# Performance work log

Hardware: AMD Instinct MI355X
Metric: run time of the kernel (lower is better)

## Reference

```python
import jax, jax.numpy as jnp
import numpy as np

B, D, L = 4, 64, 4096  # batch, pos feature dim (=pos_learnable_dim), sequence length

def setup_inputs() -> dict:
    key = jax.random.key(0)
    k1, k2 = jax.random.split(key, 2)
    pos_embed = jax.random.normal(k1, (B, D, L), dtype=jnp.float32)
    # _LinearWithBias(D, D): torch weight [out, in], bias [out]
    W_pos = (jax.random.normal(k2, (D, D), dtype=jnp.float32) / np.float32(np.sqrt(D)))
    b_pos = jnp.zeros((D,), dtype=jnp.float32)
    SOFTPLUS0 = 0.6931472  # softplus(0) = ln 2, gpytorch default raw param -> constrained value
    lengthscale = jnp.asarray(SOFTPLUS0, dtype=jnp.float32)   # RBFKernel lengthscale
    outputscale = jnp.asarray(SOFTPLUS0, dtype=jnp.float32)   # ScaleKernel outputscale
    return {"pos_embed": pos_embed, "W_pos": W_pos, "b_pos": b_pos,
            "lengthscale": lengthscale, "outputscale": outputscale}

def reference(pos_embed, W_pos, b_pos, lengthscale, outputscale):
    # pos_embed: [B, D, L]
    x = jnp.swapaxes(pos_embed, 1, 2)          # [B, L, D] (transpose, linear, transpose back, transpose again)
    x = x @ W_pos.T + b_pos                    # learnable positional linear on feature dim
    # gpytorch ScaleKernel(RBFKernel): outputscale * exp(-0.5 * ||(x_i - x_j)/lengthscale||^2)
    xs = x / lengthscale                       # [B, L, D]
    sq = jnp.sum(xs * xs, axis=-1)             # [B, L]
    sq_dist = sq[:, :, None] + sq[:, None, :] - 2.0 * jnp.einsum('bld,bmd->blm', xs, xs)
    sq_dist = jnp.maximum(sq_dist, 0.0)        # gpytorch clamps sq dist at 0
    return outputscale * jnp.exp(-0.5 * sq_dist)  # [B, L, L]
```

## Files before the change

kernel.cpp:

```cpp
#include <hip/hip_runtime.h>

using bf16x8 = __attribute__((ext_vector_type(8))) __bf16;
using f32x16 = __attribute__((ext_vector_type(16))) float;

#define BB 4
#define DD 64
#define LL 4096

__global__ __launch_bounds__(256) void prep_kernel(
    const float* __restrict__ pe,
    const float* __restrict__ W,
    const float* __restrict__ bias,
    const float* __restrict__ ls,
    __bf16* __restrict__ xs,
    float* __restrict__ h)
{
    __shared__ float pe_lds[DD][64];
    __shared__ float W_lds[DD * DD];
    __shared__ float hpart[4][64];

    const int tid = threadIdx.x;
    const int blk = blockIdx.x;
    const int b  = blk >> 6;
    const int l0 = (blk & 63) * 64;

    {
        const int l = tid & 63;
        const int kb = tid >> 6;
        #pragma unroll
        for (int it = 0; it < 16; ++it) {
            const int k = it * 4 + kb;
            pe_lds[k][l] = pe[((size_t)b * DD + k) * LL + l0 + l];
        }
    }
    #pragma unroll
    for (int it = 0; it < 16; ++it)
        W_lds[it * 256 + tid] = W[it * 256 + tid];
    __syncthreads();

    const int w = tid >> 6;
    const int l = tid & 63;
    const float inv_ls = 1.0f / ls[0];

    float acc[16];
    #pragma unroll
    for (int i = 0; i < 16; ++i) acc[i] = bias[w * 16 + i];

    for (int k4 = 0; k4 < 16; ++k4) {
        const float p0 = pe_lds[k4 * 4 + 0][l];
        const float p1 = pe_lds[k4 * 4 + 1][l];
        const float p2 = pe_lds[k4 * 4 + 2][l];
        const float p3 = pe_lds[k4 * 4 + 3][l];
        #pragma unroll
        for (int i = 0; i < 16; ++i) {
            const float4 wv = *(const float4*)&W_lds[(w * 16 + i) * DD + k4 * 4];
            acc[i] += p0 * wv.x + p1 * wv.y + p2 * wv.z + p3 * wv.w;
        }
    }

    unsigned short out16[16];
    float hs = 0.0f;
    #pragma unroll
    for (int i = 0; i < 16; ++i) {
        const float xf = acc[i] * inv_ls;
        const __bf16 bv = (__bf16)xf;
        const float xr = (float)bv;
        hs += xr * xr;
        out16[i] = __builtin_bit_cast(unsigned short, bv);
    }
    {
        __bf16* dst = xs + ((size_t)b * LL + l0 + l) * DD + w * 16;
        *(uint4*)dst       = *(const uint4*)&out16[0];
        *(uint4*)(dst + 8) = *(const uint4*)&out16[8];
    }
    hpart[w][l] = hs;
    __syncthreads();
    if (tid < 64) {
        const float s = hpart[0][tid] + hpart[1][tid] + hpart[2][tid] + hpart[3][tid];
        h[(size_t)b * LL + l0 + tid] = 0.5f * s;
    }
}

__global__ __launch_bounds__(256) void gram_kernel(
    const __bf16* __restrict__ xs,
    const float* __restrict__ h,
    const float* __restrict__ osc,
    float* __restrict__ out)
{
    const int bid = blockIdx.x;
    const int b  = bid >> 10;
    const int t  = bid & 1023;
    const int ti = t >> 5, tj = t & 31;

    const int tid  = threadIdx.x;
    const int wid  = tid >> 6;
    const int lane = tid & 63;
    const int lr = lane & 31, lg = lane >> 5;

    const int rows0 = ti * 128 + (wid >> 1) * 64;
    const int cols0 = tj * 128 + (wid & 1) * 64;

    const __bf16* xsb = xs + (size_t)b * LL * DD;
    const float*  hb  = h + (size_t)b * LL;

    bf16x8 af[2][4], bg[2][4];
    #pragma unroll
    for (int mt = 0; mt < 2; ++mt)
        #pragma unroll
        for (int kk = 0; kk < 4; ++kk)
            af[mt][kk] = *(const bf16x8*)(xsb + (size_t)(rows0 + mt * 32 + lr) * DD + kk * 16 + lg * 8);
    #pragma unroll
    for (int nt = 0; nt < 2; ++nt)
        #pragma unroll
        for (int kk = 0; kk < 4; ++kk)
            bg[nt][kk] = *(const bf16x8*)(xsb + (size_t)(cols0 + nt * 32 + lr) * DD + kk * 16 + lg * 8);

    f32x16 acc[2][2];
    #pragma unroll
    for (int mt = 0; mt < 2; ++mt)
        #pragma unroll
        for (int nt = 0; nt < 2; ++nt)
            acc[mt][nt] = (f32x16)(0.0f);

    #pragma unroll
    for (int kk = 0; kk < 4; ++kk)
        #pragma unroll
        for (int mt = 0; mt < 2; ++mt)
            #pragma unroll
            for (int nt = 0; nt < 2; ++nt)
                acc[mt][nt] = __builtin_amdgcn_mfma_f32_32x32x16_bf16(
                    af[mt][kk], bg[nt][kk], acc[mt][nt], 0, 0, 0);

    const float c = osc[0];
    const float LOG2E = 1.4426950408889634f;

    #pragma unroll
    for (int mt = 0; mt < 2; ++mt) {
        float hi[16];
        #pragma unroll
        for (int r = 0; r < 16; ++r)
            hi[r] = hb[rows0 + mt * 32 + (r & 3) + 8 * (r >> 2) + 4 * lg];
        #pragma unroll
        for (int nt = 0; nt < 2; ++nt) {
            const int col = cols0 + nt * 32 + lr;
            const float hj = hb[col];
            #pragma unroll
            for (int r = 0; r < 16; ++r) {
                const int row = rows0 + mt * 32 + (r & 3) + 8 * (r >> 2) + 4 * lg;
                float tt = acc[mt][nt][r] - hi[r] - hj;
                tt = fminf(tt, 0.0f);
                out[((size_t)b * LL + row) * LL + col] = c * __builtin_amdgcn_exp2f(tt * LOG2E);
            }
        }
    }
}

extern "C" void kernel_launch(void* const* d_in, const int* in_sizes, int n_in,
                              void* d_out, int out_size, void* d_ws, size_t ws_size,
                              hipStream_t stream) {
    const float* pe   = (const float*)d_in[0];
    const float* W    = (const float*)d_in[1];
    const float* bias = (const float*)d_in[2];
    const float* ls   = (const float*)d_in[3];
    const float* osc  = (const float*)d_in[4];
    float* out = (float*)d_out;

    __bf16* xs = (__bf16*)d_ws;
    float*  h  = (float*)((char*)d_ws + (size_t)BB * LL * DD * 2);

    prep_kernel<<<256, 256, 0, stream>>>(pe, W, bias, ls, xs, h);
    gram_kernel<<<BB * 32 * 32, 256, 0, stream>>>(xs, h, osc, out);
}
```

Before: 63.55 us.

## Fold log2e into features, shrink gram tiles, use nontemporal output stores

Scales the projected features by sqrt(log2 e)/lengthscale so the gram epilogue can call exp2 directly, removing a multiply per output. The gram kernel now uses 128x64 tiles, one 32-row strip per wave, launching twice as many blocks with a launch-bounds occupancy hint. Output stores become nontemporal so the 256MB result stream skips cache allocation. Smaller tiles mean more redundant loads of xs per output, which should be cheap since the kernel is bound by output writes.

```diff
diff --git a/kernel.cpp b/kernel.cpp
--- a/kernel.cpp
+++ b/kernel.cpp
@@ -40,7 +40,8 @@
 
     const int w = tid >> 6;
     const int l = tid & 63;
-    const float inv_ls = 1.0f / ls[0];
+    const float SQRT_LOG2E = 1.2011224087864498f;
+    const float scale = SQRT_LOG2E / ls[0];
 
     float acc[16];
     #pragma unroll
@@ -62,7 +63,7 @@
     float hs = 0.0f;
     #pragma unroll
     for (int i = 0; i < 16; ++i) {
-        const float xf = acc[i] * inv_ls;
+        const float xf = acc[i] * scale;
         const __bf16 bv = (__bf16)xf;
         const float xr = (float)bv;
         hs += xr * xr;
@@ -77,80 +78,71 @@
     __syncthreads();
     if (tid < 64) {
         const float s = hpart[0][tid] + hpart[1][tid] + hpart[2][tid] + hpart[3][tid];
-        h[(size_t)b * LL + l0 + tid] = 0.5f * s;
+        h[(size_t)b * LL + tid + l0] = 0.5f * s;
     }
 }
 
-__global__ __launch_bounds__(256) void gram_kernel(
+__global__ __launch_bounds__(256, 4) void gram_kernel(
     const __bf16* __restrict__ xs,
     const float* __restrict__ h,
     const float* __restrict__ osc,
     float* __restrict__ out)
 {
     const int bid = blockIdx.x;
-    const int b  = bid >> 10;
-    const int t  = bid & 1023;
-    const int ti = t >> 5, tj = t & 31;
+    const int b  = bid >> 11;
+    const int t  = bid & 2047;
+    const int ti = t >> 6;
+    const int tj = t & 63;
 
     const int tid  = threadIdx.x;
     const int wid  = tid >> 6;
     const int lane = tid & 63;
     const int lr = lane & 31, lg = lane >> 5;
 
-    const int rows0 = ti * 128 + (wid >> 1) * 64;
-    const int cols0 = tj * 128 + (wid & 1) * 64;
+    const int rows0 = ti * 128 + wid * 32;
+    const int cols0 = tj * 64;
 
     const __bf16* xsb = xs + (size_t)b * LL * DD;
     const float*  hb  = h + (size_t)b * LL;
 
-    bf16x8 af[2][4], bg[2][4];
+    bf16x8 af[4], bg[2][4];
     #pragma unroll
-    for (int mt = 0; mt < 2; ++mt)
-        #pragma unroll
-        for (int kk = 0; kk < 4; ++kk)
-            af[mt][kk] = *(const bf16x8*)(xsb + (size_t)(rows0 + mt * 32 + lr) * DD + kk * 16 + lg * 8);
+    for (int kk = 0; kk < 4; ++kk)
+        af[kk] = *(const bf16x8*)(xsb + (size_t)(rows0 + lr) * DD + kk * 16 + lg * 8);
     #pragma unroll
     for (int nt = 0; nt < 2; ++nt)
         #pragma unroll
         for (int kk = 0; kk < 4; ++kk)
             bg[nt][kk] = *(const bf16x8*)(xsb + (size_t)(cols0 + nt * 32 + lr) * DD + kk * 16 + lg * 8);
 
-    f32x16 acc[2][2];
-    #pragma unroll
-    for (int mt = 0; mt < 2; ++mt)
-        #pragma unroll
-        for (int nt = 0; nt < 2; ++nt)
-            acc[mt][nt] = (f32x16)(0.0f);
+    f32x16 acc[2];
+    acc[0] = (f32x16)(0.0f);
+    acc[1] = (f32x16)(0.0f);
 
     #pragma unroll
-    for (int kk = 0; kk < 4; ++kk)
-        #pragma unroll
-        for (int mt = 0; mt < 2; ++mt)
-            #pragma unroll
-            for (int nt = 0; nt < 2; ++nt)
-                acc[mt][nt] = __builtin_amdgcn_mfma_f32_32x32x16_bf16(
-                    af[mt][kk], bg[nt][kk], acc[mt][nt], 0, 0, 0);
+    for (int kk = 0; kk < 4; ++kk) {
+        acc[0] = __builtin_amdgcn_mfma_f32_32x32x16_bf16(af[kk], bg[0][kk], acc[0], 0, 0, 0);
+        acc[1] = __builtin_amdgcn_mfma_f32_32x32x16_bf16(af[kk], bg[1][kk], acc[1], 0, 0, 0);
+    }
 
     const float c = osc[0];
-    const float LOG2E = 1.4426950408889634f;
+
+    float hi[16];
+    #pragma unroll
+    for (int r = 0; r < 16; ++r)
+        hi[r] = hb[rows0 + (r & 3) + 8 * (r >> 2) + 4 * lg];
 
     #pragma unroll
-    for (int mt = 0; mt < 2; ++mt) {
-        float hi[16];
+    for (int nt = 0; nt < 2; ++nt) {
+        const int col = cols0 + nt * 32 + lr;
+        const float hj = hb[col];
         #pragma unroll
-        for (int r = 0; r < 16; ++r)
-            hi[r] = hb[rows0 + mt * 32 + (r & 3) + 8 * (r >> 2) + 4 * lg];
-        #pragma unroll
-        for (int nt = 0; nt < 2; ++nt) {
-            const int col = cols0 + nt * 32 + lr;
-            const float hj = hb[col];
-            #pragma unroll
-            for (int r = 0; r < 16; ++r) {
-                const int row = rows0 + mt * 32 + (r & 3) + 8 * (r >> 2) + 4 * lg;
-                float tt = acc[mt][nt][r] - hi[r] - hj;
-                tt = fminf(tt, 0.0f);
-                out[((size_t)b * LL + row) * LL + col] = c * __builtin_amdgcn_exp2f(tt * LOG2E);
-            }
+        for (int r = 0; r < 16; ++r) {
+            const int row = rows0 + (r & 3) + 8 * (r >> 2) + 4 * lg;
+            float tt = acc[nt][r] - hi[r] - hj;
+            tt = fminf(tt, 0.0f);
+            const float v = c * __builtin_amdgcn_exp2f(tt);
+            __builtin_nontemporal_store(v, &out[((size_t)b * LL + row) * LL + col]);
         }
     }
 }
@@ -169,5 +161,5 @@
     float*  h  = (float*)((char*)d_ws + (size_t)BB * LL * DD * 2);
 
     prep_kernel<<<256, 256, 0, stream>>>(pe, W, bias, ls, xs, h);
-    gram_kernel<<<BB * 32 * 32, 256, 0, stream>>>(xs, h, osc, out);
+    gram_kernel<<<BB * 32 * 64, 256, 0, stream>>>(xs, h, osc, out);
 }
```

Result: slower. 73.02 us (+14.9%).
